# Kernel optimization log

Hardware: AMD Instinct MI355X
Metric: run time of the kernel (lower is better)

Reference implementation:

```python
import jax, jax.numpy as jnp
import numpy as np

EPS_SCALE = 1.0
EPS_MIN = 1e-08
SOLVER_ITER = 50


def _solve_qp_simplex(M, n_iter=SOLVER_ITER):
    # Frank-Wolfe on the simplex: min_{alpha in simplex} alpha^T M alpha
    B, K, _ = M.shape
    alpha0 = jnp.full((B, K), 1.0 / K, dtype=M.dtype)

    def body(i, alpha):
        grad = 2.0 * jnp.einsum('bkj,bj->bk', M, alpha)  # (B,K)
        idx = jnp.argmin(grad, axis=1)                    # (B,)
        s = jax.nn.one_hot(idx, K, dtype=alpha.dtype)     # vertex of simplex
        step = 2.0 / (i + 2.0)
        return (1.0 - step) * alpha + step * s

    return jax.lax.fori_loop(0, n_iter, body, alpha0)


def setup_inputs() -> dict:
    key = jax.random.key(0)
    k1, k2, k3 = jax.random.split(key, 3)
    B, K = 4096, 128
    scores = jax.random.normal(k1, (B, K), dtype=jnp.float32)
    C = jax.random.uniform(k2, (B, K, K), dtype=jnp.float32)
    targets = jax.random.randint(k3, (B,), 0, K)
    return {"scores": scores, "C": C, "targets": targets}


def reference(scores, C, targets):
    B, K = scores.shape
    # eps = off-diagonal mean of C per example, scaled and clamped
    eps = (jnp.sum(C, axis=(1, 2)) - jnp.trace(C, axis1=1, axis2=2)) / (K * (K - 1))
    eps = jnp.maximum(EPS_SCALE * eps, EPS_MIN)  # (B,)
    # pairwise exponent kernel: -(f_i + f_j + C_ij)/eps, stabilized by per-example max
    exponent = -(scores[:, :, None] + scores[:, None, :] + C) / eps[:, None, None]
    shift = jnp.max(exponent, axis=(1, 2), keepdims=True)  # (B,1,1)
    M = jnp.exp(exponent - shift)  # (B,K,K)
    # inner simplex solve is NOT differentiated through (implicit FY loss)
    alpha = jax.lax.stop_gradient(_solve_qp_simplex(M, SOLVER_ITER))  # (B,K)
    val = jnp.einsum('bi,bij,bj->b', alpha, M, alpha)  # (B,)
    conjugate = -eps * (jnp.log(val + 1e-12) + shift.reshape(-1))
    f_y = jnp.take_along_axis(scores, targets[:, None], axis=1)[:, 0]
    return jnp.mean(conjugate - f_y)
```

## Files before the change

kernel.cpp:

```cpp
#include <hip/hip_runtime.h>
#include <hip/hip_bf16.h>

#define K 128
#define NB 4096
#define STRIDE_H 130
#define FW_ITERS 50

template<int CTRL>
__device__ __forceinline__ float dpp_fmin(float v) {
    int iv = __float_as_int(v);
    int s = __builtin_amdgcn_update_dpp(iv, iv, CTRL, 0xF, 0xF, false);
    return fminf(v, __int_as_float(s));
}

__device__ __forceinline__ float wave_fmin_all(float v) {
    v = dpp_fmin<0xB1>(v);
    v = dpp_fmin<0x4E>(v);
    v = dpp_fmin<0x124>(v);
    v = dpp_fmin<0x128>(v);
#if __has_builtin(__builtin_amdgcn_permlane16_swap)
    {
        auto r = __builtin_amdgcn_permlane16_swap(__float_as_int(v), __float_as_int(v), false, false);
        v = fminf(__int_as_float(r[0]), __int_as_float(r[1]));
    }
#else
    v = fminf(v, __shfl_xor(v, 16, 64));
#endif
#if __has_builtin(__builtin_amdgcn_permlane32_swap)
    {
        auto r = __builtin_amdgcn_permlane32_swap(__float_as_int(v), __float_as_int(v), false, false);
        v = fminf(__int_as_float(r[0]), __int_as_float(r[1]));
    }
#else
    v = fminf(v, __shfl_xor(v, 32, 64));
#endif
    return v;
}

__global__ __launch_bounds__(256) void cacis_main(
    const float* __restrict__ scores,
    const float* __restrict__ C,
    const int* __restrict__ targets,
    float* __restrict__ out_partial)
{
    __shared__ float s_lds[K];
    __shared__ float alpha[K];
    __shared__ float grow[K];
    __shared__ float grow2[256];
    __shared__ __hip_bfloat16 Mh[K * STRIDE_H];
    __shared__ float red[4][4];

    const int b = blockIdx.x;
    const int tid = threadIdx.x;
    const int w = tid >> 6;
    const int lane = tid & 63;

    if (tid < K) s_lds[tid] = scores[b * K + tid];
    __syncthreads();

    const float* Cb = C + (size_t)b * (K * K);
    const int cbase = 4 * (tid & 31);
    float4 c[16];
    float sc[4];
    {
        float4 s4 = *reinterpret_cast<const float4*>(&s_lds[cbase]);
        sc[0] = s4.x; sc[1] = s4.y; sc[2] = s4.z; sc[3] = s4.w;
    }

    #pragma unroll
    for (int j = 0; j < 16; ++j)
        c[j] = *reinterpret_cast<const float4*>(Cb + 4 * tid + 1024 * j);

    float sumC = 0.f, trace = 0.f, minv = 1e30f;
    #pragma unroll
    for (int j = 0; j < 16; ++j) {
        const int row = 8 * j + (tid >> 5);
        const float sr = s_lds[row];
        float4 v = c[j];
        sumC += (v.x + v.y) + (v.z + v.w);
        const int d = row - cbase;
        if (d >= 0 && d < 4)
            trace += (d == 0) ? v.x : (d == 1) ? v.y : (d == 2) ? v.z : v.w;
        float t0 = sr + sc[0] + v.x;
        float t1 = sr + sc[1] + v.y;
        float t2 = sr + sc[2] + v.z;
        float t3 = sr + sc[3] + v.w;
        c[j] = make_float4(t0, t1, t2, t3);
        minv = fminf(minv, fminf(fminf(t0, t1), fminf(t2, t3)));
    }

    #pragma unroll
    for (int m = 1; m < 64; m <<= 1) {
        sumC  += __shfl_xor(sumC, m, 64);
        trace += __shfl_xor(trace, m, 64);
        minv   = fminf(minv, __shfl_xor(minv, m, 64));
    }
    if (lane == 0) { red[w][0] = sumC; red[w][1] = trace; red[w][2] = minv; }
    __syncthreads();
    sumC  = (red[0][0] + red[1][0]) + (red[2][0] + red[3][0]);
    trace = (red[0][1] + red[1][1]) + (red[2][1] + red[3][1]);
    minv  = fminf(fminf(red[0][2], red[1][2]), fminf(red[2][2], red[3][2]));

    float eps = (sumC - trace) * (1.0f / (float)(K * (K - 1)));
    eps = fmaxf(eps, 1e-8f);
    const float inv_eps = 1.0f / eps;

    #pragma unroll
    for (int j = 0; j < 16; ++j) {
        const int row = 8 * j + (tid >> 5);
        float4 v = c[j];
        float m0 = __expf((minv - v.x) * inv_eps);
        float m1 = __expf((minv - v.y) * inv_eps);
        float m2 = __expf((minv - v.z) * inv_eps);
        float m3 = __expf((minv - v.w) * inv_eps);
        c[j] = make_float4(m0, m1, m2, m3);
        __hip_bfloat162* mp = reinterpret_cast<__hip_bfloat162*>(&Mh[row * STRIDE_H + cbase]);
        mp[0] = __hip_bfloat162(__float2bfloat16(m0), __float2bfloat16(m1));
        mp[1] = __hip_bfloat162(__float2bfloat16(m2), __float2bfloat16(m3));
    }
    __syncthreads();

    {
        const int row = tid >> 1;
        const int half = tid & 1;
        const __hip_bfloat162* rp =
            reinterpret_cast<const __hip_bfloat162*>(&Mh[row * STRIDE_H + half * 64]);
        float acc = 0.f;
        #pragma unroll
        for (int k2 = 0; k2 < 32; ++k2) {
            float2 f = __bfloat1622float2(rp[k2]);
            acc += f.x + f.y;
        }
        grow2[tid] = acc;
    }
    __syncthreads();
    if (tid < K) grow[tid] = (grow2[2 * tid] + grow2[2 * tid + 1]) * (1.0f / (float)K);
    __syncthreads();

    if (w == 0) {
        float g0 = grow[2 * lane], g1 = grow[2 * lane + 1];
        float a0 = 1.0f / K, a1 = 1.0f / K;
        #pragma unroll 1
        for (int it = 0; it < FW_ITERS; ++it) {
            const float v = wave_fmin_all(fminf(g0, g1));
            unsigned long long b0 = __ballot(g0 == v);
            unsigned long long b1 = __ballot(g1 == v);
            int i0 = b0 ? 2 * (int)__builtin_ctzll(b0)     : 0x7fffffff;
            int i1 = b1 ? 2 * (int)__builtin_ctzll(b1) + 1 : 0x7fffffff;
            const int idx = min(i0, i1);

            const float step = 2.0f / (float)(it + 2);
            const float om = 1.0f - step;
            a0 *= om; a1 *= om;
            if (2 * lane == idx)     a0 += step;
            if (2 * lane + 1 == idx) a1 += step;
            const float c0 = __bfloat162float(Mh[(2 * lane) * STRIDE_H + idx]);
            const float c1 = __bfloat162float(Mh[(2 * lane + 1) * STRIDE_H + idx]);
            g0 = om * g0 + step * c0;
            g1 = om * g1 + step * c1;
        }
        alpha[2 * lane]     = a0;
        alpha[2 * lane + 1] = a1;
    }
    __syncthreads();

    const float4 ac4 = *reinterpret_cast<const float4*>(&alpha[cbase]);
    float valp = 0.f;
    #pragma unroll
    for (int j = 0; j < 16; ++j) {
        const int row = 8 * j + (tid >> 5);
        const float4 v = c[j];
        const float dot = v.x * ac4.x + v.y * ac4.y + v.z * ac4.z + v.w * ac4.w;
        valp += alpha[row] * dot;
    }
    #pragma unroll
    for (int m = 1; m < 64; m <<= 1) valp += __shfl_xor(valp, m, 64);
    if (lane == 0) red[w][3] = valp;
    __syncthreads();
    if (tid == 0) {
        const float val = (red[0][3] + red[1][3]) + (red[2][3] + red[3][3]);
        const float conj = -eps * logf(val + 1e-12f) + minv;
        const int tgt = targets[b];
        out_partial[b] = conj - s_lds[tgt];
    }
}

__global__ __launch_bounds__(256) void cacis_reduce(
    const float* __restrict__ part, float* __restrict__ out)
{
    __shared__ float red[4];
    const int tid = threadIdx.x;
    float acc = 0.f;
    for (int i = tid; i < NB; i += 256) acc += part[i];
    #pragma unroll
    for (int m = 1; m < 64; m <<= 1) acc += __shfl_xor(acc, m, 64);
    if ((tid & 63) == 0) red[tid >> 6] = acc;
    __syncthreads();
    if (tid == 0) out[0] = ((red[0] + red[1]) + (red[2] + red[3])) * (1.0f / (float)NB);
}

extern "C" void kernel_launch(void* const* d_in, const int* in_sizes, int n_in,
                              void* d_out, int out_size, void* d_ws, size_t ws_size,
                              hipStream_t stream) {
    const float* scores  = (const float*)d_in[0];
    const float* C       = (const float*)d_in[1];
    const int*   targets = (const int*)d_in[2];
    float* out  = (float*)d_out;
    float* part = (float*)d_ws;

    cacis_main<<<NB, 256, 0, stream>>>(scores, C, targets, part);
    cacis_reduce<<<1, 256, 0, stream>>>(part, out);
}
```

Measured before the change: 82.41 us.

## Process two examples per block with parallel Frank-Wolfe waves and transposed bf16 M

Each block now handles two examples. Both M matrices are stored transposed in LDS as bf16, and two waves run the serial Frank-Wolfe loops at the same time, so the single-wave solve no longer leaves three waves idle. Row sums are computed with DPP reductions during the exp pass, and the final quadratic form is recomputed from bf16 LDS instead of fp32 registers. The cost is roughly double the LDS per block, serialized load phases for the two examples, scattered 16-bit transposed LDS writes, and lower accuracy in the final value.

```diff
diff --git a/kernel.cpp b/kernel.cpp
--- a/kernel.cpp
+++ b/kernel.cpp
@@ -3,14 +3,18 @@
 
 #define K 128
 #define NB 4096
-#define STRIDE_H 130
+#define STRIDE 130
 #define FW_ITERS 50
 
 template<int CTRL>
 __device__ __forceinline__ float dpp_fmin(float v) {
-    int iv = __float_as_int(v);
-    int s = __builtin_amdgcn_update_dpp(iv, iv, CTRL, 0xF, 0xF, false);
+    int s = __builtin_amdgcn_update_dpp(__float_as_int(v), __float_as_int(v), CTRL, 0xF, 0xF, false);
     return fminf(v, __int_as_float(s));
+}
+template<int CTRL>
+__device__ __forceinline__ float dpp_fadd(float v) {
+    int s = __builtin_amdgcn_update_dpp(__float_as_int(v), __float_as_int(v), CTRL, 0xF, 0xF, false);
+    return v + __int_as_float(s);
 }
 
 __device__ __forceinline__ float wave_fmin_all(float v) {
@@ -37,108 +41,120 @@
     return v;
 }
 
+__device__ __forceinline__ float half_sum32(float v) {
+    v = dpp_fadd<0xB1>(v);
+    v = dpp_fadd<0x4E>(v);
+    v = dpp_fadd<0x124>(v);
+    v = dpp_fadd<0x128>(v);
+#if __has_builtin(__builtin_amdgcn_permlane16_swap)
+    {
+        auto r = __builtin_amdgcn_permlane16_swap(__float_as_int(v), __float_as_int(v), false, false);
+        v = __int_as_float(r[0]) + __int_as_float(r[1]);
+    }
+#else
+    v = v + __shfl_xor(v, 16, 64);
+#endif
+    return v;
+}
+
+__device__ __forceinline__ unsigned short bf16_bits(float f) {
+    __hip_bfloat16 h = __float2bfloat16(f);
+    return *reinterpret_cast<unsigned short*>(&h);
+}
+
 __global__ __launch_bounds__(256) void cacis_main(
     const float* __restrict__ scores,
     const float* __restrict__ C,
     const int* __restrict__ targets,
     float* __restrict__ out_partial)
 {
-    __shared__ float s_lds[K];
-    __shared__ float alpha[K];
-    __shared__ float grow[K];
-    __shared__ float grow2[256];
-    __shared__ __hip_bfloat16 Mh[K * STRIDE_H];
+    __shared__ float s_lds[2][K];
+    __shared__ float alpha[2][K];
+    __shared__ float grow[2][K];
+    __shared__ unsigned short Mh[2][K * STRIDE];
     __shared__ float red[4][4];
 
     const int b = blockIdx.x;
     const int tid = threadIdx.x;
     const int w = tid >> 6;
     const int lane = tid & 63;
-
-    if (tid < K) s_lds[tid] = scores[b * K + tid];
-    __syncthreads();
-
-    const float* Cb = C + (size_t)b * (K * K);
     const int cbase = 4 * (tid & 31);
-    float4 c[16];
-    float sc[4];
-    {
-        float4 s4 = *reinterpret_cast<const float4*>(&s_lds[cbase]);
-        sc[0] = s4.x; sc[1] = s4.y; sc[2] = s4.z; sc[3] = s4.w;
-    }
-
-    #pragma unroll
-    for (int j = 0; j < 16; ++j)
-        c[j] = *reinterpret_cast<const float4*>(Cb + 4 * tid + 1024 * j);
-
-    float sumC = 0.f, trace = 0.f, minv = 1e30f;
-    #pragma unroll
-    for (int j = 0; j < 16; ++j) {
-        const int row = 8 * j + (tid >> 5);
-        const float sr = s_lds[row];
-        float4 v = c[j];
-        sumC += (v.x + v.y) + (v.z + v.w);
-        const int d = row - cbase;
-        if (d >= 0 && d < 4)
-            trace += (d == 0) ? v.x : (d == 1) ? v.y : (d == 2) ? v.z : v.w;
-        float t0 = sr + sc[0] + v.x;
-        float t1 = sr + sc[1] + v.y;
-        float t2 = sr + sc[2] + v.z;
-        float t3 = sr + sc[3] + v.w;
-        c[j] = make_float4(t0, t1, t2, t3);
-        minv = fminf(minv, fminf(fminf(t0, t1), fminf(t2, t3)));
-    }
-
-    #pragma unroll
-    for (int m = 1; m < 64; m <<= 1) {
-        sumC  += __shfl_xor(sumC, m, 64);
-        trace += __shfl_xor(trace, m, 64);
-        minv   = fminf(minv, __shfl_xor(minv, m, 64));
-    }
-    if (lane == 0) { red[w][0] = sumC; red[w][1] = trace; red[w][2] = minv; }
-    __syncthreads();
-    sumC  = (red[0][0] + red[1][0]) + (red[2][0] + red[3][0]);
-    trace = (red[0][1] + red[1][1]) + (red[2][1] + red[3][1]);
-    minv  = fminf(fminf(red[0][2], red[1][2]), fminf(red[2][2], red[3][2]));
-
-    float eps = (sumC - trace) * (1.0f / (float)(K * (K - 1)));
-    eps = fmaxf(eps, 1e-8f);
-    const float inv_eps = 1.0f / eps;
-
-    #pragma unroll
-    for (int j = 0; j < 16; ++j) {
-        const int row = 8 * j + (tid >> 5);
-        float4 v = c[j];
-        float m0 = __expf((minv - v.x) * inv_eps);
-        float m1 = __expf((minv - v.y) * inv_eps);
-        float m2 = __expf((minv - v.z) * inv_eps);
-        float m3 = __expf((minv - v.w) * inv_eps);
-        c[j] = make_float4(m0, m1, m2, m3);
-        __hip_bfloat162* mp = reinterpret_cast<__hip_bfloat162*>(&Mh[row * STRIDE_H + cbase]);
-        mp[0] = __hip_bfloat162(__float2bfloat16(m0), __float2bfloat16(m1));
-        mp[1] = __hip_bfloat162(__float2bfloat16(m2), __float2bfloat16(m3));
-    }
-    __syncthreads();
-
-    {
-        const int row = tid >> 1;
-        const int half = tid & 1;
-        const __hip_bfloat162* rp =
-            reinterpret_cast<const __hip_bfloat162*>(&Mh[row * STRIDE_H + half * 64]);
-        float acc = 0.f;
-        #pragma unroll
-        for (int k2 = 0; k2 < 32; ++k2) {
-            float2 f = __bfloat1622float2(rp[k2]);
-            acc += f.x + f.y;
-        }
-        grow2[tid] = acc;
-    }
-    __syncthreads();
-    if (tid < K) grow[tid] = (grow2[2 * tid] + grow2[2 * tid + 1]) * (1.0f / (float)K);
-    __syncthreads();
-
-    if (w == 0) {
-        float g0 = grow[2 * lane], g1 = grow[2 * lane + 1];
+
+    float eps_e[2], minv_e[2];
+
+    for (int e = 0; e < 2; ++e) {
+        const int ex = 2 * b + e;
+        if (tid < K) s_lds[e][tid] = scores[ex * K + tid];
+        __syncthreads();
+
+        const float* Cb = C + (size_t)ex * (K * K);
+        float4 c[16];
+        #pragma unroll
+        for (int j = 0; j < 16; ++j)
+            c[j] = *reinterpret_cast<const float4*>(Cb + 4 * tid + 1024 * j);
+
+        float sc[4];
+        {
+            float4 s4 = *reinterpret_cast<const float4*>(&s_lds[e][cbase]);
+            sc[0] = s4.x; sc[1] = s4.y; sc[2] = s4.z; sc[3] = s4.w;
+        }
+
+        float sumC = 0.f, trace = 0.f, minv = 1e30f;
+        #pragma unroll
+        for (int j = 0; j < 16; ++j) {
+            const int row = 8 * j + (tid >> 5);
+            const float sr = s_lds[e][row];
+            float4 v = c[j];
+            sumC += (v.x + v.y) + (v.z + v.w);
+            const int d = row - cbase;
+            if (d >= 0 && d < 4)
+                trace += (d == 0) ? v.x : (d == 1) ? v.y : (d == 2) ? v.z : v.w;
+            float t0 = sr + sc[0] + v.x;
+            float t1 = sr + sc[1] + v.y;
+            float t2 = sr + sc[2] + v.z;
+            float t3 = sr + sc[3] + v.w;
+            c[j] = make_float4(t0, t1, t2, t3);
+            minv = fminf(minv, fminf(fminf(t0, t1), fminf(t2, t3)));
+        }
+
+        #pragma unroll
+        for (int m = 1; m < 64; m <<= 1) {
+            sumC  += __shfl_xor(sumC, m, 64);
+            trace += __shfl_xor(trace, m, 64);
+            minv   = fminf(minv, __shfl_xor(minv, m, 64));
+        }
+        if (lane == 0) { red[w][0] = sumC; red[w][1] = trace; red[w][2] = minv; }
+        __syncthreads();
+        sumC  = (red[0][0] + red[1][0]) + (red[2][0] + red[3][0]);
+        trace = (red[0][1] + red[1][1]) + (red[2][1] + red[3][1]);
+        minv  = fminf(fminf(red[0][2], red[1][2]), fminf(red[2][2], red[3][2]));
+
+        float eps = (sumC - trace) * (1.0f / (float)(K * (K - 1)));
+        eps = fmaxf(eps, 1e-8f);
+        const float inv_eps = 1.0f / eps;
+        eps_e[e] = eps; minv_e[e] = minv;
+
+        #pragma unroll
+        for (int j = 0; j < 16; ++j) {
+            const int row = 8 * j + (tid >> 5);
+            float4 v = c[j];
+            float m0 = __expf((minv - v.x) * inv_eps);
+            float m1 = __expf((minv - v.y) * inv_eps);
+            float m2 = __expf((minv - v.z) * inv_eps);
+            float m3 = __expf((minv - v.w) * inv_eps);
+            Mh[e][(cbase + 0) * STRIDE + row] = bf16_bits(m0);
+            Mh[e][(cbase + 1) * STRIDE + row] = bf16_bits(m1);
+            Mh[e][(cbase + 2) * STRIDE + row] = bf16_bits(m2);
+            Mh[e][(cbase + 3) * STRIDE + row] = bf16_bits(m3);
+            float rs = half_sum32((m0 + m1) + (m2 + m3));
+            if ((lane & 31) == 0) grow[e][row] = rs * (1.0f / (float)K);
+        }
+        __syncthreads();
+    }
+
+    if (w < 2) {
+        const unsigned short* mb = &Mh[w][0];
+        float g0 = grow[w][2 * lane], g1 = grow[w][2 * lane + 1];
         float a0 = 1.0f / K, a1 = 1.0f / K;
         #pragma unroll 1
         for (int it = 0; it < FW_ITERS; ++it) {
@@ -154,34 +170,42 @@
             a0 *= om; a1 *= om;
             if (2 * lane == idx)     a0 += step;
             if (2 * lane + 1 == idx) a1 += step;
-            const float c0 = __bfloat162float(Mh[(2 * lane) * STRIDE_H + idx]);
-            const float c1 = __bfloat162float(Mh[(2 * lane + 1) * STRIDE_H + idx]);
+            unsigned int u = *reinterpret_cast<const unsigned int*>(&mb[idx * STRIDE + 2 * lane]);
+            float c0 = __uint_as_float(u << 16);
+            float c1 = __uint_as_float(u & 0xffff0000u);
             g0 = om * g0 + step * c0;
             g1 = om * g1 + step * c1;
         }
-        alpha[2 * lane]     = a0;
-        alpha[2 * lane + 1] = a1;
+        alpha[w][2 * lane]     = a0;
+        alpha[w][2 * lane + 1] = a1;
     }
     __syncthreads();
 
-    const float4 ac4 = *reinterpret_cast<const float4*>(&alpha[cbase]);
-    float valp = 0.f;
-    #pragma unroll
-    for (int j = 0; j < 16; ++j) {
-        const int row = 8 * j + (tid >> 5);
-        const float4 v = c[j];
-        const float dot = v.x * ac4.x + v.y * ac4.y + v.z * ac4.z + v.w * ac4.w;
-        valp += alpha[row] * dot;
-    }
-    #pragma unroll
-    for (int m = 1; m < 64; m <<= 1) valp += __shfl_xor(valp, m, 64);
-    if (lane == 0) red[w][3] = valp;
-    __syncthreads();
-    if (tid == 0) {
-        const float val = (red[0][3] + red[1][3]) + (red[2][3] + red[3][3]);
-        const float conj = -eps * logf(val + 1e-12f) + minv;
-        const int tgt = targets[b];
-        out_partial[b] = conj - s_lds[tgt];
+    for (int e = 0; e < 2; ++e) {
+        const int col = tid >> 1;
+        const int rh  = tid & 1;
+        const unsigned short* cp = &Mh[e][col * STRIDE + rh * 64];
+        const float ac = alpha[e][col];
+        float acc = 0.f;
+        #pragma unroll
+        for (int k = 0; k < 32; ++k) {
+            unsigned int u = *reinterpret_cast<const unsigned int*>(&cp[2 * k]);
+            float m0 = __uint_as_float(u << 16);
+            float m1 = __uint_as_float(u & 0xffff0000u);
+            acc += alpha[e][rh * 64 + 2 * k] * m0 + alpha[e][rh * 64 + 2 * k + 1] * m1;
+        }
+        float valp = acc * ac;
+        #pragma unroll
+        for (int m = 1; m < 64; m <<= 1) valp += __shfl_xor(valp, m, 64);
+        if (lane == 0) red[w][0] = valp;
+        __syncthreads();
+        if (tid == 0) {
+            const float val = (red[0][0] + red[1][0]) + (red[2][0] + red[3][0]);
+            const float conj = -eps_e[e] * logf(val + 1e-12f) + minv_e[e];
+            const int tgt = targets[2 * b + e];
+            out_partial[2 * b + e] = conj - s_lds[e][tgt];
+        }
+        __syncthreads();
     }
 }
 
@@ -208,6 +232,6 @@
     float* out  = (float*)d_out;
     float* part = (float*)d_ws;
 
-    cacis_main<<<NB, 256, 0, stream>>>(scores, C, targets, part);
+    cacis_main<<<NB / 2, 256, 0, stream>>>(scores, C, targets, part);
     cacis_reduce<<<1, 256, 0, stream>>>(part, out);
 }
```

New measurement: 120.7 us. 46.4% more time.
